# Kernel tuning notes

Measured on AMD Instinct MI355X. Metric: run time of the kernel, lower is better.

## Reference

```python
import jax
import jax.numpy as jnp
from jax import lax
import numpy as np

IN_SCALE, IN_ZP = 0.01, 7
W_SCALE, W_ZP = 0.01, 3
B_SCALE = 0.0001
I32_MIN, I32_MAX = -(2.0**31), 2.0**31 - 1


def setup_inputs() -> dict:
    key = jax.random.key(0)
    k1, k2, k3 = jax.random.split(key, 3)
    # int8 quantized input activations and weights (torch passes torch.int8 tensors)
    inputVec = jax.random.randint(k1, (32, 128, 56, 56), -128, 128, dtype=jnp.int32).astype(jnp.int8)
    weight = jax.random.randint(k2, (256, 128, 3, 3), -128, 128, dtype=jnp.int32).astype(jnp.int8)
    bias = jax.random.normal(k3, (256,), dtype=jnp.float32)
    return {"inputVec": inputVec, "weight": weight, "bias": bias}


def reference(inputVec, weight, bias):
    # dequantize per-tensor: (q - zero_point) * scale
    x = (inputVec.astype(jnp.float32) - IN_ZP) * IN_SCALE   # [N, Cin, H, W]
    w = (weight.astype(jnp.float32) - W_ZP) * W_SCALE       # [Cout, Cin, kh, kw]
    # quantize bias to qint32 (round-half-even, clamp to int32 range) then dequantize
    b = jnp.clip(jnp.round(bias / B_SCALE), I32_MIN, I32_MAX) * B_SCALE  # [Cout]
    # conv2d: stride 1, no padding, dilation 1, groups 1
    out = lax.conv_general_dilated(
        x, w,
        window_strides=(1, 1),
        padding='VALID',
        dimension_numbers=('NCHW', 'OIHW', 'NCHW'),
    )  # [N, Cout, H-2, W-2]
    return out + b[None, :, None, None]
```

## Files before the change

### kernel.cpp

```cpp
#include <hip/hip_runtime.h>
#include <hip/hip_bf16.h>


#define N_B   32
#define C_IN  128
#define H_IN  56
#define W_IN  56
#define C_OUT 256
#define H_OUT 54
#define W_OUT 54
#define K_TOT 1152
#define NPX   (N_B * H_OUT * W_OUT)
#define PXROW (H_OUT * W_OUT)

using i32x4  = __attribute__((ext_vector_type(4))) int;

static __device__ __forceinline__ int dot4(int a, int b, int c) {
#if __has_builtin(__builtin_amdgcn_sdot4)
  return __builtin_amdgcn_sdot4(a, b, c, false);
#else
  signed char a0 = (signed char)a, a1 = (signed char)(a >> 8),
              a2 = (signed char)(a >> 16), a3 = (signed char)(a >> 24);
  signed char b0 = (signed char)b, b1 = (signed char)(b >> 8),
              b2 = (signed char)(b >> 16), b3 = (signed char)(b >> 24);
  return c + a0 * b0 + a1 * b1 + a2 * b2 + a3 * b3;
#endif
}

__device__ __forceinline__ void gload16(const void* g, void* l) {
  __builtin_amdgcn_global_load_lds(
      (const __attribute__((address_space(1))) void*)g,
      (__attribute__((address_space(3))) void*)l, 16, 0, 0);
}

__global__ void repack_w(const int* __restrict__ w, const float* __restrict__ bias,
                         signed char* __restrict__ wq3, float* __restrict__ bconst) {
  int co = blockIdx.x;
  int ci = threadIdx.x;
  const int* wrow = w + (size_t)co * K_TOT + (size_t)ci * 9;
  int s = 0;
  int kk = ci >> 5, h = (ci >> 4) & 1, b = ci & 15;
  size_t base = (size_t)kk * 8192 + h * 4096 + co * 16 + b;
#pragma unroll
  for (int t = 0; t < 9; ++t) {
    int v = wrow[t];
    s += v;
    wq3[(size_t)t * 32768 + base] = (signed char)v;
  }
  __shared__ int red[128];
  red[ci] = s;
  __syncthreads();
  for (int off = 64; off > 0; off >>= 1) {
    if (ci < off) red[ci] += red[ci + off];
    __syncthreads();
  }
  if (ci == 0) {
    int wsum = red[0];
    float r = rintf(bias[co] / 0.0001f);
    r = fminf(fmaxf(r, -2147483648.0f), 2147483647.0f);
    bconst[co] = 1e-4f * (float)(-7 * wsum + 24192) + r * 0.0001f;
  }
}

__global__ void repack_in(const int* __restrict__ in, signed char* __restrict__ ip2,
                          int* __restrict__ rs) {
  __shared__ int t32[C_IN * W_IN];
  __shared__ int rsum[W_IN];
  int h = blockIdx.x, n = blockIdx.y;
  int tid = threadIdx.x;
  if (tid < W_IN) rsum[tid] = 0;

  int ci = tid >> 1, hf = tid & 1;
  const int* s = in + ((size_t)n * C_IN + ci) * (H_IN * W_IN) + h * W_IN + hf * 28;
  int* d = &t32[ci * W_IN + hf * 28];
#pragma unroll
  for (int k = 0; k < 7; ++k)
    *(int4*)(d + k * 4) = *(const int4*)(s + k * 4);
  __syncthreads();

  signed char* dst = ip2 + ((size_t)n * H_IN + h) * 8192;
#pragma unroll
  for (int jj = 0; jj < 2; ++jj) {
    int j = jj * 256 + tid;
    int q = j >> 6, w = j & 63;
    if (w < W_IN) {
      int b[4], srow = 0;
#pragma unroll
      for (int qq = 0; qq < 4; ++qq) {
        int x0 = t32[(q * 16 + qq * 4 + 0) * W_IN + w];
        int x1 = t32[(q * 16 + qq * 4 + 1) * W_IN + w];
        int x2 = t32[(q * 16 + qq * 4 + 2) * W_IN + w];
        int x3 = t32[(q * 16 + qq * 4 + 3) * W_IN + w];
        b[qq] = (x0 & 255) | ((x1 & 255) << 8) | ((x2 & 255) << 16) | ((x3 & 255) << 24);
        srow = dot4(b[qq], 0x01010101, srow);
      }
      *(int4*)(dst + (size_t)q * 1024 + w * 16) = *(int4*)b;
      atomicAdd(&rsum[w], srow);
    }
  }
  __syncthreads();
  if (tid < W_IN) rs[((size_t)n * H_IN + h) * W_IN + tid] = rsum[tid];
}

__global__ void asum_k(const int* __restrict__ rs, float* __restrict__ asumf) {
  int px = blockIdx.x * 256 + threadIdx.x;
  if (px >= NPX) return;
  int n = px / PXROW, rem = px - n * PXROW;
  int y = rem / W_OUT, x = rem - y * W_OUT;
  const int* rp = rs + ((size_t)n * H_IN + y) * W_IN + x;
  int s = 0;
#pragma unroll
  for (int kh = 0; kh < 3; ++kh)
    s += rp[kh * W_IN + 0] + rp[kh * W_IN + 1] + rp[kh * W_IN + 2];
  asumf[px] = -3e-4f * (float)s;
}

__device__ __forceinline__ int mklb(int pf, int pxl, int c16) {
  int j = pf * 16 + pxl;
  int jc = j > 107 ? 107 : j;
  int dy = (jc >= 54) ? 1 : 0;
  return c16 * 4096 + dy * 1024 + (jc - dy * 54) * 16;
}

__launch_bounds__(256, 4)
__global__ void conv_mfma(const signed char* __restrict__ ip2,
                          const signed char* __restrict__ wq3,
                          const float* __restrict__ asumf,
                          const float* __restrict__ bconst,
                          float* __restrict__ out) {
  __shared__ signed char lds[32768];
  const int tid = threadIdx.x, w = tid >> 6, l = tid & 63;
  const int c16 = l >> 4, pxl = l & 15;

  const int b0 = blockIdx.x;
  const int wg = (b0 & 7) * 216 + (b0 >> 3);
  const int cq = wg & 1;
  const int nr = wg >> 1;
  const int n  = nr / 27;
  const int rp = nr - n * 27;
  const int y0 = rp * 2;

  const signed char* ipn = ip2 + ((size_t)n * H_IN + y0) * 8192;
  {
    const int r = tid >> 6;
    const int off = (tid & 63) * 16;
    const signed char* src = ipn + (size_t)r * 8192 + off;
#pragma unroll
    for (int i = 0; i < 8; ++i)
      gload16(src + (size_t)i * 1024, &lds[i * 4096 + tid * 16]);
  }

  const int lb0 = mklb(0, pxl, c16), lb1 = mklb(1, pxl, c16), lb2 = mklb(2, pxl, c16),
            lb3 = mklb(3, pxl, c16), lb4 = mklb(4, pxl, c16), lb5 = mklb(5, pxl, c16),
            lb6 = mklb(6, pxl, c16);

  const signed char* awq = wq3 + (size_t)c16 * 4096 +
                           (size_t)(cq * 128 + w * 32 + pxl) * 16;

  i32x4 a0_0 = {0,0,0,0}, a0_1 = {0,0,0,0}, a0_2 = {0,0,0,0}, a0_3 = {0,0,0,0},
        a0_4 = {0,0,0,0}, a0_5 = {0,0,0,0}, a0_6 = {0,0,0,0};
  i32x4 a1_0 = {0,0,0,0}, a1_1 = {0,0,0,0}, a1_2 = {0,0,0,0}, a1_3 = {0,0,0,0},
        a1_4 = {0,0,0,0}, a1_5 = {0,0,0,0}, a1_6 = {0,0,0,0};
  i32x4 wa0, wa1, wb0, wb1;

#define LDW(P, t)                                                              \
  P##0 = *(const i32x4*)(awq + (size_t)(t) * 16384);                           \
  P##1 = *(const i32x4*)(awq + (size_t)(t) * 16384 + 256);

  LDW(wa, 0);
  __syncthreads();

#define KSTEP(ks, U, L, DOLOAD)                                                \
  {                                                                            \
    if (DOLOAD) { LDW(L, (ks) + 1); }                                          \
    __builtin_amdgcn_sched_barrier(0);                                         \
    constexpr int d_ = ((ks) & 1) * 16384 + (((ks) >> 1) / 3) * 1024 +         \
                       (((ks) >> 1) % 3) * 16;                                 \
    i32x4 q0 = *(const i32x4*)(&lds[lb0 + d_]);                                \
    i32x4 q1 = *(const i32x4*)(&lds[lb1 + d_]);                                \
    i32x4 q2 = *(const i32x4*)(&lds[lb2 + d_]);                                \
    i32x4 q3 = *(const i32x4*)(&lds[lb3 + d_]);                                \
    i32x4 q4 = *(const i32x4*)(&lds[lb4 + d_]);                                \
    i32x4 q5 = *(const i32x4*)(&lds[lb5 + d_]);                                \
    i32x4 q6 = *(const i32x4*)(&lds[lb6 + d_]);                                \
    __builtin_amdgcn_s_setprio(1);                                             \
    a0_0 = __builtin_amdgcn_mfma_i32_16x16x64_i8(U##0, q0, a0_0, 0, 0, 0);     \
    a1_0 = __builtin_amdgcn_mfma_i32_16x16x64_i8(U##1, q0, a1_0, 0, 0, 0);     \
    a0_1 = __builtin_amdgcn_mfma_i32_16x16x64_i8(U##0, q1, a0_1, 0, 0, 0);     \
    a1_1 = __builtin_amdgcn_mfma_i32_16x16x64_i8(U##1, q1, a1_1, 0, 0, 0);     \
    a0_2 = __builtin_amdgcn_mfma_i32_16x16x64_i8(U##0, q2, a0_2, 0, 0, 0);     \
    a1_2 = __builtin_amdgcn_mfma_i32_16x16x64_i8(U##1, q2, a1_2, 0, 0, 0);     \
    a0_3 = __builtin_amdgcn_mfma_i32_16x16x64_i8(U##0, q3, a0_3, 0, 0, 0);     \
    a1_3 = __builtin_amdgcn_mfma_i32_16x16x64_i8(U##1, q3, a1_3, 0, 0, 0);     \
    a0_4 = __builtin_amdgcn_mfma_i32_16x16x64_i8(U##0, q4, a0_4, 0, 0, 0);     \
    a1_4 = __builtin_amdgcn_mfma_i32_16x16x64_i8(U##1, q4, a1_4, 0, 0, 0);     \
    a0_5 = __builtin_amdgcn_mfma_i32_16x16x64_i8(U##0, q5, a0_5, 0, 0, 0);     \
    a1_5 = __builtin_amdgcn_mfma_i32_16x16x64_i8(U##1, q5, a1_5, 0, 0, 0);     \
    a0_6 = __builtin_amdgcn_mfma_i32_16x16x64_i8(U##0, q6, a0_6, 0, 0, 0);     \
    a1_6 = __builtin_amdgcn_mfma_i32_16x16x64_i8(U##1, q6, a1_6, 0, 0, 0);     \
    __builtin_amdgcn_s_setprio(0);                                             \
  }

  KSTEP(0,  wa, wb, 1)  KSTEP(1,  wb, wa, 1)  KSTEP(2,  wa, wb, 1)
  KSTEP(3,  wb, wa, 1)  KSTEP(4,  wa, wb, 1)  KSTEP(5,  wb, wa, 1)
  KSTEP(6,  wa, wb, 1)  KSTEP(7,  wb, wa, 1)  KSTEP(8,  wa, wb, 1)
  KSTEP(9,  wb, wa, 1)  KSTEP(10, wa, wb, 1)  KSTEP(11, wb, wa, 1)
  KSTEP(12, wa, wb, 1)  KSTEP(13, wb, wa, 1)  KSTEP(14, wa, wb, 1)
  KSTEP(15, wb, wa, 1)  KSTEP(16, wa, wb, 1)  KSTEP(17, wb, wa, 0)
#undef KSTEP
#undef LDW

  float* obase = out + ((size_t)n * C_OUT + cq * 128) * PXROW + y0 * W_OUT;
  const float* apx = asumf + (size_t)n * PXROW + y0 * W_OUT;
  const float asf0 = apx[pxl];
  const float asf1 = apx[16 + pxl];
  const float asf2 = apx[32 + pxl];
  const float asf3 = apx[48 + pxl];
  const float asf4 = apx[64 + pxl];
  const float asf5 = apx[80 + pxl];
  const int j6 = 96 + pxl;
  const float asf6 = (j6 < 108) ? apx[j6] : 0.0f;
#pragma unroll
  for (int m = 0; m < 2; ++m) {
#pragma unroll
    for (int j = 0; j < 4; ++j) {
      int co = w * 32 + m * 16 + c16 * 4 + j;
      float bc = bconst[cq * 128 + co];
      float* o = obase + (size_t)co * PXROW;
      const i32x4& v0 = m ? a1_0 : a0_0;
      const i32x4& v1 = m ? a1_1 : a0_1;
      const i32x4& v2 = m ? a1_2 : a0_2;
      const i32x4& v3 = m ? a1_3 : a0_3;
      const i32x4& v4 = m ? a1_4 : a0_4;
      const i32x4& v5 = m ? a1_5 : a0_5;
      const i32x4& v6 = m ? a1_6 : a0_6;
      o[pxl]      = 1e-4f * (float)v0[j] + asf0 + bc;
      o[16 + pxl] = 1e-4f * (float)v1[j] + asf1 + bc;
      o[32 + pxl] = 1e-4f * (float)v2[j] + asf2 + bc;
      o[48 + pxl] = 1e-4f * (float)v3[j] + asf3 + bc;
      o[64 + pxl] = 1e-4f * (float)v4[j] + asf4 + bc;
      o[80 + pxl] = 1e-4f * (float)v5[j] + asf5 + bc;
      if (j6 < 108)
        o[j6] = 1e-4f * (float)v6[j] + asf6 + bc;
    }
  }
}

__global__ void conv_naive(const int* __restrict__ in, const int* __restrict__ w,
                           const float* __restrict__ bias, float* __restrict__ out) {
  size_t idx = (size_t)blockIdx.x * 256 + threadIdx.x;
  size_t total = (size_t)N_B * C_OUT * H_OUT * W_OUT;
  if (idx >= total) return;
  int x = idx % W_OUT; size_t t = idx / W_OUT;
  int y = t % H_OUT; t /= H_OUT;
  int co = t % C_OUT; int n = (int)(t / C_OUT);
  int acc = 0;
  for (int ci = 0; ci < C_IN; ++ci) {
    const int* ib = in + (((size_t)n * C_IN + ci) * H_IN + y) * W_IN + x;
    const int* wb = w + (((size_t)co * C_IN + ci) * 3) * 3;
    for (int kh = 0; kh < 3; ++kh)
      for (int kw = 0; kw < 3; ++kw)
        acc += (ib[kh * W_IN + kw] - 7) * (wb[kh * 3 + kw] - 3);
  }
  float r = rintf(bias[co] / 0.0001f);
  r = fminf(fmaxf(r, -2147483648.0f), 2147483647.0f);
  out[idx] = (float)acc * (0.01f * 0.01f) + r * 0.0001f;
}

extern "C" void kernel_launch(void* const* d_in, const int* in_sizes, int n_in,
                              void* d_out, int out_size, void* d_ws, size_t ws_size,
                              hipStream_t stream) {
  const int*   in   = (const int*)d_in[0];
  const int*   w    = (const int*)d_in[1];
  const float* bias = (const float*)d_in[2];
  float*       out  = (float*)d_out;

  const size_t WQ_OFF = 0;
  const size_t IP_OFF = 294912;
  const size_t RS_OFF = IP_OFF + 14680064;
  const size_t AF_OFF = RS_OFF + 401408;
  const size_t BC_OFF = AF_OFF + 373248;
  const size_t NEED   = BC_OFF + 1024;

  if (ws_size >= NEED) {
    char* ws = (char*)d_ws;
    signed char* wq3  = (signed char*)(ws + WQ_OFF);
    signed char* ip2  = (signed char*)(ws + IP_OFF);
    int*         rs   = (int*)(ws + RS_OFF);
    float*       af   = (float*)(ws + AF_OFF);
    float*       bc   = (float*)(ws + BC_OFF);

    repack_w<<<C_OUT, 128, 0, stream>>>(w, bias, wq3, bc);
    repack_in<<<dim3(H_IN, N_B), 256, 0, stream>>>(in, ip2, rs);
    asum_k<<<(NPX + 255) / 256, 256, 0, stream>>>(rs, af);
    conv_mfma<<<1728, 256, 0, stream>>>(ip2, wq3, af, bc, out);
  } else {
    size_t total = (size_t)N_B * C_OUT * H_OUT * W_OUT;
    conv_naive<<<(total + 255) / 256, 256, 0, stream>>>(in, w, bias, out);
  }
}
```

Before: 56.21 us.

## Merge prep kernels into one launch and compute activation sums inside conv

Combines the weight repack and input repack kernels into a single launch that chooses its role by block index. It drops the separate activation-sum kernel by having each conv block compute its 108 per-pixel sums from the row sums into shared memory. It also splits each K-step's LDS loads and MFMAs into two scheduling groups so fewer operand registers are live at once. This saves two kernel launches and an intermediate buffer round trip, but adds a small amount of redundant global reads and a little more LDS per conv block.

```diff
diff --git a/kernel.cpp b/kernel.cpp
--- a/kernel.cpp
+++ b/kernel.cpp
@@ -33,86 +33,74 @@
       (__attribute__((address_space(3))) void*)l, 16, 0, 0);
 }
 
-__global__ void repack_w(const int* __restrict__ w, const float* __restrict__ bias,
-                         signed char* __restrict__ wq3, float* __restrict__ bconst) {
-  int co = blockIdx.x;
-  int ci = threadIdx.x;
-  const int* wrow = w + (size_t)co * K_TOT + (size_t)ci * 9;
-  int s = 0;
-  int kk = ci >> 5, h = (ci >> 4) & 1, b = ci & 15;
-  size_t base = (size_t)kk * 8192 + h * 4096 + co * 16 + b;
-#pragma unroll
-  for (int t = 0; t < 9; ++t) {
-    int v = wrow[t];
-    s += v;
-    wq3[(size_t)t * 32768 + base] = (signed char)v;
-  }
-  __shared__ int red[128];
-  red[ci] = s;
-  __syncthreads();
-  for (int off = 64; off > 0; off >>= 1) {
-    if (ci < off) red[ci] += red[ci + off];
-    __syncthreads();
-  }
-  if (ci == 0) {
-    int wsum = red[0];
-    float r = rintf(bias[co] / 0.0001f);
-    r = fminf(fmaxf(r, -2147483648.0f), 2147483647.0f);
-    bconst[co] = 1e-4f * (float)(-7 * wsum + 24192) + r * 0.0001f;
-  }
-}
-
-__global__ void repack_in(const int* __restrict__ in, signed char* __restrict__ ip2,
-                          int* __restrict__ rs) {
+__global__ void prep(const int* __restrict__ in, const int* __restrict__ wsrc,
+                     const float* __restrict__ bias,
+                     signed char* __restrict__ ip2, int* __restrict__ rs,
+                     signed char* __restrict__ wq3, float* __restrict__ bconst) {
+  const int bid = blockIdx.x, tid = threadIdx.x;
   __shared__ int t32[C_IN * W_IN];
   __shared__ int rsum[W_IN];
-  int h = blockIdx.x, n = blockIdx.y;
-  int tid = threadIdx.x;
-  if (tid < W_IN) rsum[tid] = 0;
-
-  int ci = tid >> 1, hf = tid & 1;
-  const int* s = in + ((size_t)n * C_IN + ci) * (H_IN * W_IN) + h * W_IN + hf * 28;
-  int* d = &t32[ci * W_IN + hf * 28];
-#pragma unroll
-  for (int k = 0; k < 7; ++k)
-    *(int4*)(d + k * 4) = *(const int4*)(s + k * 4);
-  __syncthreads();
-
-  signed char* dst = ip2 + ((size_t)n * H_IN + h) * 8192;
-#pragma unroll
-  for (int jj = 0; jj < 2; ++jj) {
-    int j = jj * 256 + tid;
-    int q = j >> 6, w = j & 63;
-    if (w < W_IN) {
-      int b[4], srow = 0;
-#pragma unroll
-      for (int qq = 0; qq < 4; ++qq) {
-        int x0 = t32[(q * 16 + qq * 4 + 0) * W_IN + w];
-        int x1 = t32[(q * 16 + qq * 4 + 1) * W_IN + w];
-        int x2 = t32[(q * 16 + qq * 4 + 2) * W_IN + w];
-        int x3 = t32[(q * 16 + qq * 4 + 3) * W_IN + w];
-        b[qq] = (x0 & 255) | ((x1 & 255) << 8) | ((x2 & 255) << 16) | ((x3 & 255) << 24);
-        srow = dot4(b[qq], 0x01010101, srow);
+
+  if (bid < 1792) {
+    const int h = bid % 56, n = bid / 56;
+    if (tid < W_IN) rsum[tid] = 0;
+    int ci = tid >> 1, hf = tid & 1;
+    const int* s = in + ((size_t)n * C_IN + ci) * (H_IN * W_IN) + h * W_IN + hf * 28;
+    int* d = &t32[ci * W_IN + hf * 28];
+#pragma unroll
+    for (int k = 0; k < 7; ++k)
+      *(int4*)(d + k * 4) = *(const int4*)(s + k * 4);
+    __syncthreads();
+
+    signed char* dst = ip2 + ((size_t)n * H_IN + h) * 8192;
+#pragma unroll
+    for (int jj = 0; jj < 2; ++jj) {
+      int j = jj * 256 + tid;
+      int q = j >> 6, w = j & 63;
+      if (w < W_IN) {
+        int b[4], srow = 0;
+#pragma unroll
+        for (int qq = 0; qq < 4; ++qq) {
+          int x0 = t32[(q * 16 + qq * 4 + 0) * W_IN + w];
+          int x1 = t32[(q * 16 + qq * 4 + 1) * W_IN + w];
+          int x2 = t32[(q * 16 + qq * 4 + 2) * W_IN + w];
+          int x3 = t32[(q * 16 + qq * 4 + 3) * W_IN + w];
+          b[qq] = (x0 & 255) | ((x1 & 255) << 8) | ((x2 & 255) << 16) | ((x3 & 255) << 24);
+          srow = dot4(b[qq], 0x01010101, srow);
+        }
+        *(int4*)(dst + (size_t)q * 1024 + w * 16) = *(int4*)b;
+        atomicAdd(&rsum[w], srow);
       }
-      *(int4*)(dst + (size_t)q * 1024 + w * 16) = *(int4*)b;
-      atomicAdd(&rsum[w], srow);
-    }
-  }
-  __syncthreads();
-  if (tid < W_IN) rs[((size_t)n * H_IN + h) * W_IN + tid] = rsum[tid];
-}
-
-__global__ void asum_k(const int* __restrict__ rs, float* __restrict__ asumf) {
-  int px = blockIdx.x * 256 + threadIdx.x;
-  if (px >= NPX) return;
-  int n = px / PXROW, rem = px - n * PXROW;
-  int y = rem / W_OUT, x = rem - y * W_OUT;
-  const int* rp = rs + ((size_t)n * H_IN + y) * W_IN + x;
-  int s = 0;
-#pragma unroll
-  for (int kh = 0; kh < 3; ++kh)
-    s += rp[kh * W_IN + 0] + rp[kh * W_IN + 1] + rp[kh * W_IN + 2];
-  asumf[px] = -3e-4f * (float)s;
+    }
+    __syncthreads();
+    if (tid < W_IN) rs[((size_t)n * H_IN + h) * W_IN + tid] = rsum[tid];
+  } else {
+    int* red = t32;
+    const int co = (bid - 1792) * 2 + (tid >> 7);
+    const int ci = tid & 127;
+    const int* wrow = wsrc + (size_t)co * K_TOT + (size_t)ci * 9;
+    int s = 0;
+    int kk = ci >> 5, hh = (ci >> 4) & 1, b = ci & 15;
+    size_t base = (size_t)kk * 8192 + hh * 4096 + co * 16 + b;
+#pragma unroll
+    for (int t = 0; t < 9; ++t) {
+      int v = wrow[t];
+      s += v;
+      wq3[(size_t)t * 32768 + base] = (signed char)v;
+    }
+    red[tid] = s;
+    __syncthreads();
+    for (int off = 64; off > 0; off >>= 1) {
+      if (ci < off) red[tid] += red[tid + off];
+      __syncthreads();
+    }
+    if (ci == 0) {
+      int wsum = red[tid];
+      float r = rintf(bias[co] / 0.0001f);
+      r = fminf(fmaxf(r, -2147483648.0f), 2147483647.0f);
+      bconst[co] = 1e-4f * (float)(-7 * wsum + 24192) + r * 0.0001f;
+    }
+  }
 }
 
 __device__ __forceinline__ int mklb(int pf, int pxl, int c16) {
@@ -125,10 +113,11 @@
 __launch_bounds__(256, 4)
 __global__ void conv_mfma(const signed char* __restrict__ ip2,
                           const signed char* __restrict__ wq3,
-                          const float* __restrict__ asumf,
+                          const int* __restrict__ rs,
                           const float* __restrict__ bconst,
                           float* __restrict__ out) {
   __shared__ signed char lds[32768];
+  __shared__ float asf_lds[112];
   const int tid = threadIdx.x, w = tid >> 6, l = tid & 63;
   const int c16 = l >> 4, pxl = l & 15;
 
@@ -150,6 +139,17 @@
       gload16(src + (size_t)i * 1024, &lds[i * 4096 + tid * 16]);
   }
 
+  if (tid < 108) {
+    int dy = (tid >= 54) ? 1 : 0;
+    int x  = tid - dy * 54;
+    const int* rp_ = rs + ((size_t)n * H_IN + y0 + dy) * W_IN + x;
+    int s = 0;
+#pragma unroll
+    for (int kh = 0; kh < 3; ++kh)
+      s += rp_[kh * W_IN + 0] + rp_[kh * W_IN + 1] + rp_[kh * W_IN + 2];
+    asf_lds[tid] = -3e-4f * (float)s;
+  }
+
   const int lb0 = mklb(0, pxl, c16), lb1 = mklb(1, pxl, c16), lb2 = mklb(2, pxl, c16),
             lb3 = mklb(3, pxl, c16), lb4 = mklb(4, pxl, c16), lb5 = mklb(5, pxl, c16),
             lb6 = mklb(6, pxl, c16);
@@ -176,29 +176,36 @@
     __builtin_amdgcn_sched_barrier(0);                                         \
     constexpr int d_ = ((ks) & 1) * 16384 + (((ks) >> 1) / 3) * 1024 +         \
                        (((ks) >> 1) % 3) * 16;                                 \
-    i32x4 q0 = *(const i32x4*)(&lds[lb0 + d_]);                                \
-    i32x4 q1 = *(const i32x4*)(&lds[lb1 + d_]);                                \
-    i32x4 q2 = *(const i32x4*)(&lds[lb2 + d_]);                                \
-    i32x4 q3 = *(const i32x4*)(&lds[lb3 + d_]);                                \
-    i32x4 q4 = *(const i32x4*)(&lds[lb4 + d_]);                                \
-    i32x4 q5 = *(const i32x4*)(&lds[lb5 + d_]);                                \
-    i32x4 q6 = *(const i32x4*)(&lds[lb6 + d_]);                                \
-    __builtin_amdgcn_s_setprio(1);                                             \
-    a0_0 = __builtin_amdgcn_mfma_i32_16x16x64_i8(U##0, q0, a0_0, 0, 0, 0);     \
-    a1_0 = __builtin_amdgcn_mfma_i32_16x16x64_i8(U##1, q0, a1_0, 0, 0, 0);     \
-    a0_1 = __builtin_amdgcn_mfma_i32_16x16x64_i8(U##0, q1, a0_1, 0, 0, 0);     \
-    a1_1 = __builtin_amdgcn_mfma_i32_16x16x64_i8(U##1, q1, a1_1, 0, 0, 0);     \
-    a0_2 = __builtin_amdgcn_mfma_i32_16x16x64_i8(U##0, q2, a0_2, 0, 0, 0);     \
-    a1_2 = __builtin_amdgcn_mfma_i32_16x16x64_i8(U##1, q2, a1_2, 0, 0, 0);     \
-    a0_3 = __builtin_amdgcn_mfma_i32_16x16x64_i8(U##0, q3, a0_3, 0, 0, 0);     \
-    a1_3 = __builtin_amdgcn_mfma_i32_16x16x64_i8(U##1, q3, a1_3, 0, 0, 0);     \
-    a0_4 = __builtin_amdgcn_mfma_i32_16x16x64_i8(U##0, q4, a0_4, 0, 0, 0);     \
-    a1_4 = __builtin_amdgcn_mfma_i32_16x16x64_i8(U##1, q4, a1_4, 0, 0, 0);     \
-    a0_5 = __builtin_amdgcn_mfma_i32_16x16x64_i8(U##0, q5, a0_5, 0, 0, 0);     \
-    a1_5 = __builtin_amdgcn_mfma_i32_16x16x64_i8(U##1, q5, a1_5, 0, 0, 0);     \
-    a0_6 = __builtin_amdgcn_mfma_i32_16x16x64_i8(U##0, q6, a0_6, 0, 0, 0);     \
-    a1_6 = __builtin_amdgcn_mfma_i32_16x16x64_i8(U##1, q6, a1_6, 0, 0, 0);     \
-    __builtin_amdgcn_s_setprio(0);                                             \
+    {                                                                          \
+      i32x4 q0 = *(const i32x4*)(&lds[lb0 + d_]);                              \
+      i32x4 q1 = *(const i32x4*)(&lds[lb1 + d_]);                              \
+      i32x4 q2 = *(const i32x4*)(&lds[lb2 + d_]);                              \
+      i32x4 q3 = *(const i32x4*)(&lds[lb3 + d_]);                              \
+      __builtin_amdgcn_s_setprio(1);                                           \
+      a0_0 = __builtin_amdgcn_mfma_i32_16x16x64_i8(U##0, q0, a0_0, 0, 0, 0);   \
+      a1_0 = __builtin_amdgcn_mfma_i32_16x16x64_i8(U##1, q0, a1_0, 0, 0, 0);   \
+      a0_1 = __builtin_amdgcn_mfma_i32_16x16x64_i8(U##0, q1, a0_1, 0, 0, 0);   \
+      a1_1 = __builtin_amdgcn_mfma_i32_16x16x64_i8(U##1, q1, a1_1, 0, 0, 0);   \
+      a0_2 = __builtin_amdgcn_mfma_i32_16x16x64_i8(U##0, q2, a0_2, 0, 0, 0);   \
+      a1_2 = __builtin_amdgcn_mfma_i32_16x16x64_i8(U##1, q2, a1_2, 0, 0, 0);   \
+      a0_3 = __builtin_amdgcn_mfma_i32_16x16x64_i8(U##0, q3, a0_3, 0, 0, 0);   \
+      a1_3 = __builtin_amdgcn_mfma_i32_16x16x64_i8(U##1, q3, a1_3, 0, 0, 0);   \
+      __builtin_amdgcn_s_setprio(0);                                           \
+    }                                                                          \
+    __builtin_amdgcn_sched_barrier(0);                                         \
+    {                                                                          \
+      i32x4 q4 = *(const i32x4*)(&lds[lb4 + d_]);                              \
+      i32x4 q5 = *(const i32x4*)(&lds[lb5 + d_]);                              \
+      i32x4 q6 = *(const i32x4*)(&lds[lb6 + d_]);                              \
+      __builtin_amdgcn_s_setprio(1);                                           \
+      a0_4 = __builtin_amdgcn_mfma_i32_16x16x64_i8(U##0, q4, a0_4, 0, 0, 0);   \
+      a1_4 = __builtin_amdgcn_mfma_i32_16x16x64_i8(U##1, q4, a1_4, 0, 0, 0);   \
+      a0_5 = __builtin_amdgcn_mfma_i32_16x16x64_i8(U##0, q5, a0_5, 0, 0, 0);   \
+      a1_5 = __builtin_amdgcn_mfma_i32_16x16x64_i8(U##1, q5, a1_5, 0, 0, 0);   \
+      a0_6 = __builtin_amdgcn_mfma_i32_16x16x64_i8(U##0, q6, a0_6, 0, 0, 0);   \
+      a1_6 = __builtin_amdgcn_mfma_i32_16x16x64_i8(U##1, q6, a1_6, 0, 0, 0);   \
+      __builtin_amdgcn_s_setprio(0);                                           \
+    }                                                                          \
   }
 
   KSTEP(0,  wa, wb, 1)  KSTEP(1,  wb, wa, 1)  KSTEP(2,  wa, wb, 1)
@@ -211,15 +218,14 @@
 #undef LDW
 
   float* obase = out + ((size_t)n * C_OUT + cq * 128) * PXROW + y0 * W_OUT;
-  const float* apx = asumf + (size_t)n * PXROW + y0 * W_OUT;
-  const float asf0 = apx[pxl];
-  const float asf1 = apx[16 + pxl];
-  const float asf2 = apx[32 + pxl];
-  const float asf3 = apx[48 + pxl];
-  const float asf4 = apx[64 + pxl];
-  const float asf5 = apx[80 + pxl];
+  const float asf0 = asf_lds[pxl];
+  const float asf1 = asf_lds[16 + pxl];
+  const float asf2 = asf_lds[32 + pxl];
+  const float asf3 = asf_lds[48 + pxl];
+  const float asf4 = asf_lds[64 + pxl];
+  const float asf5 = asf_lds[80 + pxl];
   const int j6 = 96 + pxl;
-  const float asf6 = (j6 < 108) ? apx[j6] : 0.0f;
+  const float asf6 = (j6 < 108) ? asf_lds[j6] : 0.0f;
 #pragma unroll
   for (int m = 0; m < 2; ++m) {
 #pragma unroll
@@ -278,8 +284,7 @@
   const size_t WQ_OFF = 0;
   const size_t IP_OFF = 294912;
   const size_t RS_OFF = IP_OFF + 14680064;
-  const size_t AF_OFF = RS_OFF + 401408;
-  const size_t BC_OFF = AF_OFF + 373248;
+  const size_t BC_OFF = RS_OFF + 401408;
   const size_t NEED   = BC_OFF + 1024;
 
   if (ws_size >= NEED) {
@@ -287,13 +292,10 @@
     signed char* wq3  = (signed char*)(ws + WQ_OFF);
     signed char* ip2  = (signed char*)(ws + IP_OFF);
     int*         rs   = (int*)(ws + RS_OFF);
-    float*       af   = (float*)(ws + AF_OFF);
     float*       bc   = (float*)(ws + BC_OFF);
 
-    repack_w<<<C_OUT, 128, 0, stream>>>(w, bias, wq3, bc);
-    repack_in<<<dim3(H_IN, N_B), 256, 0, stream>>>(in, ip2, rs);
-    asum_k<<<(NPX + 255) / 256, 256, 0, stream>>>(rs, af);
-    conv_mfma<<<1728, 256, 0, stream>>>(ip2, wq3, af, bc, out);
+    prep<<<1920, 256, 0, stream>>>(in, w, bias, ip2, rs, wq3, bc);
+    conv_mfma<<<1728, 256, 0, stream>>>(ip2, wq3, rs, bc, out);
   } else {
     size_t total = (size_t)N_B * C_OUT * H_OUT * W_OUT;
     conv_naive<<<(total + 255) / 256, 256, 0, stream>>>(in, w, bias, out);
```

Result: faster. 50.48 us (-10.2%).
